# Kernel optimization log

Measured on AMD Instinct MI355X. Metric: run time of the kernel, lower is better.

The kernel has to match this reference:

```python
import jax, jax.numpy as jnp
import numpy as np

NEG_INF = -1e30

def _rotate_half(x):
    x1, x2 = jnp.split(x, 2, axis=-1)
    return jnp.concatenate([-x2, x1], axis=-1)

def _apply_rope(x, sin, cos):
    # x: [b, t, h, d]; sin/cos: [t, d]
    s = sin[None, :, None, :]
    c = cos[None, :, None, :]
    return x * c + _rotate_half(x) * s

def setup_inputs() -> dict:
    key = jax.random.key(0)
    ks = jax.random.split(key, 5)
    B, T, D, H = 2, 2048, 2048, 16
    hd = D // H
    x = jax.random.normal(ks[0], (B, T, D), dtype=jnp.float32)
    sin = jax.random.normal(ks[1], (T, hd), dtype=jnp.float32)
    cos = jax.random.normal(ks[2], (T, hd), dtype=jnp.float32)
    W_qkv = jax.random.normal(ks[3], (D, D + 2 * hd), dtype=jnp.float32) * (1.0 / np.sqrt(D))
    W_o = jax.random.normal(ks[4], (D, D), dtype=jnp.float32) * (1.0 / np.sqrt(D))
    return {"x": x, "sin": sin, "cos": cos, "W_qkv": W_qkv, "W_o": W_o}

def reference(x, sin, cos, W_qkv, W_o):
    B, T, D = x.shape
    num_heads = 16
    head_dim = D // num_heads
    scale = head_dim ** (-0.5)

    qkv = x @ W_qkv                              # [B, T, D + 2*hd]
    q, k, v = jnp.split(qkv, [D, D + head_dim], axis=-1)
    # q -> [B, H, T, hd]; k, v single KV head -> [B, 1, T, hd]
    q = q.reshape(B, T, num_heads, head_dim).transpose(0, 2, 1, 3)
    k = k[:, :, None, :].transpose(0, 2, 1, 3)   # [B, 1, T, hd]
    v = v[:, :, None, :].transpose(0, 2, 1, 3)

    # module scales q by head_dim^-0.5 BEFORE rope/attention
    q = q * scale

    # apply_rope_safe: transpose to [B, T, H, hd], apply rope, transpose back
    q = _apply_rope(q.transpose(0, 2, 1, 3), sin, cos).transpose(0, 2, 1, 3)
    k = _apply_rope(k.transpose(0, 2, 1, 3), sin, cos).transpose(0, 2, 1, 3)

    k0 = k[:, 0]                                 # [B, T, hd] (MQA shared KV)
    v0 = v[:, 0]

    # jax.nn.dot_product_attention applies its own 1/sqrt(hd) scaling on top
    scores = jnp.einsum('bhqd,bkd->bhqk', q, k0) * scale
    causal = jnp.tril(jnp.ones((T, T), dtype=bool))
    scores = jnp.where(causal[None, None], scores, NEG_INF)
    probs = jax.nn.softmax(scores, axis=-1)
    out = jnp.einsum('bhqk,bkd->bhqd', probs, v0)  # [B, H, T, hd]

    out = out.transpose(0, 2, 1, 3).reshape(B, T, D)
    return out @ W_o
```

## Files before the change

### kernel.cpp

```cpp
#include <hip/hip_runtime.h>
#include <stdint.h>

typedef __bf16 bf16x8_t __attribute__((ext_vector_type(8)));
typedef float f32x4_t __attribute__((ext_vector_type(4)));

#define AS1 __attribute__((address_space(1)))
#define AS3 __attribute__((address_space(3)))

static __device__ __forceinline__ unsigned short f2bf(float f) {
  union { float f; unsigned u; } a;
  a.f = f;
  unsigned r = a.u + 0x7fffu + ((a.u >> 16) & 1u);
  return (unsigned short)(r >> 16);
}

static __device__ __forceinline__ unsigned cvtpk(float lo, float hi) {
  unsigned r;
  asm("v_cvt_pk_bf16_f32 %0, %1, %2" : "=v"(r) : "v"(lo), "v"(hi));
  return r;
}

__global__ void cvt_bf16_kernel(const float* __restrict__ in, unsigned short* __restrict__ out) {
  long i = ((long)blockIdx.x * blockDim.x + threadIdx.x) * 4;
  float4 v = *(const float4*)(in + i);
  ushort4 o;
  o.x = f2bf(v.x);
  o.y = f2bf(v.y);
  o.z = f2bf(v.z);
  o.w = f2bf(v.w);
  *(ushort4*)(out + i) = o;
}

__global__ void transpose_f32_bf16(const float* __restrict__ src, unsigned short* __restrict__ dst,
                                   int ld, int dld, long sbs, long dbs) {
  __shared__ float tile[64][65];
  src += (long)blockIdx.z * sbs;
  dst += (long)blockIdx.z * dbs;
  const int c0 = blockIdx.x * 64, r0 = blockIdx.y * 64;
  const int tx = threadIdx.x, ty = threadIdx.y;
#pragma unroll
  for (int j = 0; j < 64; j += 4)
    tile[ty + j][tx] = src[(long)(r0 + ty + j) * ld + (c0 + tx)];
  __syncthreads();
#pragma unroll
  for (int j = 0; j < 64; j += 4)
    dst[(long)(c0 + ty + j) * dld + (r0 + tx)] = f2bf(tile[tx][ty + j]);
}

__global__ __launch_bounds__(256) void gemm_bt(const unsigned short* __restrict__ A,
                                               const unsigned short* __restrict__ Bt,
                                               float* __restrict__ C,
                                               int M, int N, int K, int nx) {
  __shared__ unsigned short As[3][128 * 32];
  __shared__ unsigned short Bs[3][128 * 32];
  const int nwg = gridDim.x;
  const int bid = blockIdx.x;
  const int swz = (bid & 7) * (nwg >> 3) + (bid >> 3);
  const int by = swz / nx;
  const int bx = swz - by * nx;

  const int tid = threadIdx.x;
  const int wid = tid >> 6, lane = tid & 63;
  const int r16 = lane & 15, g = lane >> 4;
  const long bm = (long)by * 128;
  const long bn = (long)bx * 128;
  const int wr = (wid >> 1) * 64, wc = (wid & 1) * 64;
  const int gr = g ^ (r16 & 3);
  const int sslot = (lane & 3) ^ ((lane >> 2) & 3);

  f32x4_t acc[4][4];
#pragma unroll
  for (int i = 0; i < 4; i++)
#pragma unroll
    for (int j = 0; j < 4; j++) acc[i][j] = (f32x4_t){0.f, 0.f, 0.f, 0.f};

  const int NT = K >> 5;

#define STAGE_G(buf, kt)                                                              \
  {                                                                                   \
    _Pragma("unroll") for (int i = 0; i < 2; i++) {                                   \
      const int chunk = (i * 4 + wid) * 64 + lane;                                    \
      const int row = chunk >> 2;                                                     \
      __builtin_amdgcn_global_load_lds(                                               \
          (const AS1 void*)(A + (bm + row) * K + (kt) + sslot * 8),                   \
          (AS3 void*)(&As[buf][chunk * 8]), 16, 0, 0);                                \
      __builtin_amdgcn_global_load_lds(                                               \
          (const AS1 void*)(Bt + (bn + row) * K + (kt) + sslot * 8),                  \
          (AS3 void*)(&Bs[buf][chunk * 8]), 16, 0, 0);                                \
    }                                                                                 \
  }

  STAGE_G(0, 0)
  STAGE_G(1, 32)
  asm volatile("s_waitcnt vmcnt(4)" ::: "memory");
  __builtin_amdgcn_s_barrier();

  for (int T = 0; T < NT; T++) {
    const int cur = T % 3;
    if (T + 2 < NT) {
      const int nb = (T + 2) % 3;
      STAGE_G(nb, (T + 2) * 32)
    }
    __builtin_amdgcn_sched_barrier(0);
    bf16x8_t af[4], bfr[4];
#pragma unroll
    for (int mi = 0; mi < 4; mi++)
      af[mi] = *(const bf16x8_t*)(&As[cur][(wr + mi * 16 + r16) * 32 + gr * 8]);
#pragma unroll
    for (int ni = 0; ni < 4; ni++)
      bfr[ni] = *(const bf16x8_t*)(&Bs[cur][(wc + ni * 16 + r16) * 32 + gr * 8]);
    __builtin_amdgcn_s_setprio(1);
#pragma unroll
    for (int mi = 0; mi < 4; mi++)
#pragma unroll
      for (int ni = 0; ni < 4; ni++)
        acc[mi][ni] = __builtin_amdgcn_mfma_f32_16x16x32_bf16(af[mi], bfr[ni], acc[mi][ni], 0, 0, 0);
    __builtin_amdgcn_s_setprio(0);
    if (T + 2 < NT)
      asm volatile("s_waitcnt vmcnt(4)" ::: "memory");
    else
      asm volatile("s_waitcnt vmcnt(0)" ::: "memory");
    __builtin_amdgcn_s_barrier();
  }
#undef STAGE_G

#pragma unroll
  for (int mi = 0; mi < 4; mi++)
#pragma unroll
    for (int ni = 0; ni < 4; ni++) {
      const long rowb = bm + wr + mi * 16 + 4 * g;
      const long colb = bn + wc + ni * 16 + r16;
#pragma unroll
      for (int j = 0; j < 4; j++)
        C[(rowb + j) * N + colb] = acc[mi][ni][j];
    }
}

__global__ void rope_kernel(const float* __restrict__ qkv,
                            const float* __restrict__ sinp,
                            const float* __restrict__ cosp,
                            unsigned short* __restrict__ qr,
                            unsigned short* __restrict__ kr) {
  const int row = blockIdx.x;
  const int b = row >> 11, t = row & 2047;
  const float* src = qkv + (long)row * 2304;
  const int tid = threadIdx.x;
  const int d = tid & 127;
  const int dp = (d + 64) & 127;
  const float c = cosp[t * 128 + d];
  const float s = sinp[t * 128 + d];
  const float sgn = (d < 64) ? -1.f : 1.f;
  for (int h = (tid >> 7); h < 16; h += 2) {
    const float x0 = src[h * 128 + d];
    const float xp = src[h * 128 + dp];
    qr[((long)((b * 16 + h) * 2048 + t)) * 128 + d] =
        f2bf((x0 * c + sgn * xp * s) * 0.011271055f);
  }
  if (tid < 128) {
    const float x0 = src[2048 + d];
    const float xp = src[2048 + dp];
    kr[((long)(b * 2048 + t)) * 128 + d] = f2bf(x0 * c + sgn * xp * s);
  }
}

__global__ __launch_bounds__(256, 2)
void mqa_attn(const unsigned short* __restrict__ qr,
              const unsigned short* __restrict__ kr,
              const unsigned short* __restrict__ vT,
              unsigned short* __restrict__ ao) {
  __shared__ unsigned short Kb[2][64 * 128];
  __shared__ unsigned short Vb[2][128 * 64];
  __shared__ unsigned short plds[4][16 * 64];
  const int idx = blockIdx.x;
  const int pj = idx & 15, h = (idx >> 4) & 15, b = idx >> 8;
  const int tid = threadIdx.x;
  const int wid = tid >> 6, lane = tid & 63;
  const int r = lane & 15, g = lane >> 4;
  const int rs = r & 7;
  char* pw = (char*)&plds[wid][0];

  const unsigned short* kbase = kr + (long)b * 2048 * 128;
  const unsigned short* vbase = vT + (long)b * 128 * 2048;
  const unsigned short* qh = qr + (long)(b * 16 + h) * 2048 * 128;

  const int scol = (tid & 15) ^ ((tid >> 4) & 7);
  const int vscol = (tid & 7) ^ ((tid >> 3) & 7);

  f32x4_t o[8];
#pragma unroll
  for (int i = 0; i < 8; i++) o[i] = (f32x4_t){0.f, 0.f, 0.f, 0.f};
  float m = 0.f, lsum = 0.f;

  int tile = pj;
  bf16x8_t qf[4];
  {
    const unsigned short* qp = qh + (long)(tile * 64 + wid * 16 + r) * 128 + g * 8;
#pragma unroll
    for (int c = 0; c < 4; c++) qf[c] = *(const bf16x8_t*)(qp + c * 32);
  }

#pragma unroll
  for (int i = 0; i < 4; i++) {
    const int row = i * 16 + (tid >> 4);
    __builtin_amdgcn_global_load_lds(
        (const AS1 void*)(kbase + (long)row * 128 + scol * 8),
        (AS3 void*)(&Kb[0][(i * 256 + tid) * 8]), 16, 0, 0);
  }
#pragma unroll
  for (int i = 0; i < 4; i++) {
    const int vrow = i * 32 + (tid >> 3);
    __builtin_amdgcn_global_load_lds(
        (const AS1 void*)(vbase + (long)vrow * 2048 + vscol * 8),
        (AS3 void*)(&Vb[0][(i * 256 + tid) * 8]), 16, 0, 0);
  }
  asm volatile("s_waitcnt vmcnt(0)" ::: "memory");
  __builtin_amdgcn_s_barrier();

  const int switch_s = pj + 1;
  for (int s = 0; s <= 32; s++) {
    const int cur = s & 1;

    if (s == switch_s) {
      float lt = lsum;
      lt += __shfl_xor(lt, 16);
      lt += __shfl_xor(lt, 32);
      float rl[4];
#pragma unroll
      for (int jj = 0; jj < 4; jj++) rl[jj] = 1.0f / __shfl(lt, 4 * g + jj);
      unsigned short* aop = ao + ((long)(b * 2048 + tile * 64 + wid * 16 + 4 * g)) * 2048 + h * 128 + r;
#pragma unroll
      for (int dt = 0; dt < 8; dt++)
#pragma unroll
        for (int jj = 0; jj < 4; jj++)
          aop[(long)jj * 2048 + dt * 16] = f2bf(o[dt][jj] * rl[jj]);
      tile = 31 - pj;
      const unsigned short* qp = qh + (long)(tile * 64 + wid * 16 + r) * 128 + g * 8;
#pragma unroll
      for (int c = 0; c < 4; c++) qf[c] = *(const bf16x8_t*)(qp + c * 32);
#pragma unroll
      for (int i = 0; i < 8; i++) o[i] = (f32x4_t){0.f, 0.f, 0.f, 0.f};
      m = 0.f;
      lsum = 0.f;
    }

    if (s < 32) {
      const int kvn = (s + 1 <= pj) ? 64 * (s + 1) : 64 * (s - pj);
#pragma unroll
      for (int i = 0; i < 4; i++) {
        const int row = i * 16 + (tid >> 4);
        __builtin_amdgcn_global_load_lds(
            (const AS1 void*)(kbase + (long)(kvn + row) * 128 + scol * 8),
            (AS3 void*)(&Kb[cur ^ 1][(i * 256 + tid) * 8]), 16, 0, 0);
      }
      __builtin_amdgcn_sched_barrier(0);
#pragma unroll
      for (int i = 0; i < 4; i++) {
        const int vrow = i * 32 + (tid >> 3);
        __builtin_amdgcn_global_load_lds(
            (const AS1 void*)(vbase + (long)vrow * 2048 + kvn + vscol * 8),
            (AS3 void*)(&Vb[cur ^ 1][(i * 256 + tid) * 8]), 16, 0, 0);
      }
    }
    __builtin_amdgcn_sched_barrier(0);

    f32x4_t sc[4];
#pragma unroll
    for (int t = 0; t < 4; t++) sc[t] = (f32x4_t){0.f, 0.f, 0.f, 0.f};
    const unsigned short* Kcur = &Kb[cur][0];
    __builtin_amdgcn_s_setprio(1);
#pragma unroll
    for (int t = 0; t < 4; t++) {
      const unsigned short* krow = Kcur + (16 * t + r) * 128;
#pragma unroll
      for (int c = 0; c < 4; c++) {
        const bf16x8_t kf = *(const bf16x8_t*)(krow + (((4 * c + g) ^ rs) << 3));
        sc[t] = __builtin_amdgcn_mfma_f32_16x16x32_bf16(kf, qf[c], sc[t], 0, 0, 0);
      }
    }
    __builtin_amdgcn_s_setprio(0);

    if (s == pj || s == 32) {
#pragma unroll
      for (int t = 0; t < 4; t++)
#pragma unroll
        for (int jj = 0; jj < 4; jj++)
          if (t * 16 + 4 * g + jj > wid * 16 + r) sc[t][jj] = -1e30f;
    }
    float mx01 = fmaxf(fmaxf(sc[0][0], sc[0][1]), fmaxf(sc[0][2], sc[0][3]));
    float mx23 = fmaxf(fmaxf(sc[1][0], sc[1][1]), fmaxf(sc[1][2], sc[1][3]));
    float mx45 = fmaxf(fmaxf(sc[2][0], sc[2][1]), fmaxf(sc[2][2], sc[2][3]));
    float mx67 = fmaxf(fmaxf(sc[3][0], sc[3][1]), fmaxf(sc[3][2], sc[3][3]));
    const float lm = fmaxf(fmaxf(mx01, mx23), fmaxf(mx45, mx67));
    if (!__all(lm <= m + 11.5f)) {
      float pm = lm;
      pm = fmaxf(pm, __shfl_xor(pm, 16));
      pm = fmaxf(pm, __shfl_xor(pm, 32));
      const float mnew = fmaxf(m, pm);
      const float alpha = __builtin_amdgcn_exp2f(m - mnew);
      lsum *= alpha;
      float aj[4];
#pragma unroll
      for (int jj = 0; jj < 4; jj++) aj[jj] = __shfl(alpha, 4 * g + jj);
#pragma unroll
      for (int dt = 0; dt < 8; dt++) {
        o[dt][0] *= aj[0]; o[dt][1] *= aj[1]; o[dt][2] *= aj[2]; o[dt][3] *= aj[3];
      }
      m = mnew;
    }
    float p[16];
#pragma unroll
    for (int t = 0; t < 4; t++)
#pragma unroll
      for (int jj = 0; jj < 4; jj++) p[4 * t + jj] = __builtin_amdgcn_exp2f(sc[t][jj] - m);
    float ls = 0.f;
#pragma unroll
    for (int i = 0; i < 16; i++) ls += p[i];
    lsum += ls;

    asm volatile("" ::: "memory");
#pragma unroll
    for (int t = 0; t < 4; t++) {
      uint2 w = {cvtpk(p[4 * t], p[4 * t + 1]), cvtpk(p[4 * t + 2], p[4 * t + 3])};
      *(uint2*)(pw + r * 128 + (((2 * t + (g >> 1)) ^ rs) << 4) + ((g & 1) << 3)) = w;
    }
    asm volatile("s_waitcnt lgkmcnt(0)" ::: "memory");
    const bf16x8_t pa0 = *(const bf16x8_t*)(pw + r * 128 + ((g ^ rs) << 4));
    const bf16x8_t pa1 = *(const bf16x8_t*)(pw + r * 128 + (((4 + g) ^ rs) << 4));

    if (s < 32)
      asm volatile("s_waitcnt vmcnt(8)" ::: "memory");
    else
      asm volatile("s_waitcnt vmcnt(0)" ::: "memory");
    __builtin_amdgcn_s_barrier();

    const unsigned short* Vcur = &Vb[cur][0];
    __builtin_amdgcn_s_setprio(1);
#pragma unroll
    for (int dt = 0; dt < 8; dt++) {
      const bf16x8_t vfA = *(const bf16x8_t*)(Vcur + (dt * 16 + r) * 64 + ((g ^ rs) << 3));
      o[dt] = __builtin_amdgcn_mfma_f32_16x16x32_bf16(pa0, vfA, o[dt], 0, 0, 0);
    }
#pragma unroll
    for (int dt = 0; dt < 8; dt++) {
      const bf16x8_t vfB = *(const bf16x8_t*)(Vcur + (dt * 16 + r) * 64 + (((4 + g) ^ rs) << 3));
      o[dt] = __builtin_amdgcn_mfma_f32_16x16x32_bf16(pa1, vfB, o[dt], 0, 0, 0);
    }
    __builtin_amdgcn_s_setprio(0);

    if (s < 32)
      asm volatile("s_waitcnt vmcnt(4)" ::: "memory");
    else
      asm volatile("s_waitcnt vmcnt(0)" ::: "memory");
    __builtin_amdgcn_s_barrier();
  }
  {
    float lt = lsum;
    lt += __shfl_xor(lt, 16);
    lt += __shfl_xor(lt, 32);
    float rl[4];
#pragma unroll
    for (int jj = 0; jj < 4; jj++) rl[jj] = 1.0f / __shfl(lt, 4 * g + jj);
    unsigned short* aop = ao + ((long)(b * 2048 + tile * 64 + wid * 16 + 4 * g)) * 2048 + h * 128 + r;
#pragma unroll
    for (int dt = 0; dt < 8; dt++)
#pragma unroll
      for (int jj = 0; jj < 4; jj++)
        aop[(long)jj * 2048 + dt * 16] = f2bf(o[dt][jj] * rl[jj]);
  }
}

extern "C" void kernel_launch(void* const* d_in, const int* in_sizes, int n_in,
                              void* d_out, int out_size, void* d_ws, size_t ws_size,
                              hipStream_t stream) {
  const float* x    = (const float*)d_in[0];
  const float* sinp = (const float*)d_in[1];
  const float* cosp = (const float*)d_in[2];
  const float* Wqkv = (const float*)d_in[3];
  const float* Wo   = (const float*)d_in[4];
  float* out = (float*)d_out;
  char* ws = (char*)d_ws;

  const int B = 2, T = 2048, D = 2048, H = 16, HD = 128;
  const int M = B * T;
  const int NQ = D + 2 * HD;

  unsigned short* xb    = (unsigned short*)(ws + 0);
  unsigned short* wqkvT = (unsigned short*)(ws + 16777216);
  unsigned short* woT   = (unsigned short*)(ws + 26214400);
  float*          qkv   = (float*)         (ws + 34603008);
  unsigned short* qr    = (unsigned short*)(ws + 72351744);
  unsigned short* kr    = (unsigned short*)(ws + 89128960);
  unsigned short* vT    = (unsigned short*)(ws + 90177536);
  unsigned short* ao    = xb;

  dim3 tb(64, 4);
  cvt_bf16_kernel<<<(M * D) / 1024, 256, 0, stream>>>(x, xb);
  transpose_f32_bf16<<<dim3(NQ / 64, D / 64, 1), tb, 0, stream>>>(Wqkv, wqkvT, NQ, D, 0, 0);
  transpose_f32_bf16<<<dim3(D / 64, D / 64, 1), tb, 0, stream>>>(Wo, woT, D, D, 0, 0);
  gemm_bt<<<dim3((NQ / 128) * (M / 128)), 256, 0, stream>>>(xb, wqkvT, qkv, M, NQ, D, NQ / 128);
  rope_kernel<<<M, 256, 0, stream>>>(qkv, sinp, cosp, qr, kr);
  transpose_f32_bf16<<<dim3(HD / 64, T / 64, B), tb, 0, stream>>>(
      qkv + 2176, vT, NQ, T, (long)T * NQ, (long)HD * T);
  mqa_attn<<<dim3(512), 256, 0, stream>>>(qr, kr, vT, ao);
  gemm_bt<<<dim3((D / 128) * (M / 128)), 256, 0, stream>>>(ao, woT, out, M, D, D, D / 128);
}
```

Baseline: 202.8 us.

## Fuse RoPE, scaling and V transpose into the QKV GEMM epilogue

The QKV projection GEMM now applies RoPE and the q scale in its epilogue, with each warp's column mapping paired so d and d+64 live in the same thread. It writes bf16 q/k directly and a transposed bf16 V through an LDS staging tile. This removes the fp32 qkv intermediate round trip plus the separate rope and V-transpose launches. It adds an interleaved cos/sin table kernel and a heavier epilogue with scattered float2 table reads.

```diff
diff --git a/kernel.cpp b/kernel.cpp
--- a/kernel.cpp
+++ b/kernel.cpp
@@ -18,6 +18,15 @@
   unsigned r;
   asm("v_cvt_pk_bf16_f32 %0, %1, %2" : "=v"(r) : "v"(lo), "v"(hi));
   return r;
+}
+
+__global__ void build_cs(const float* __restrict__ sinp, const float* __restrict__ cosp,
+                         float2* __restrict__ cs) {
+  const int i = blockIdx.x * 256 + threadIdx.x;
+  float2 v;
+  v.x = cosp[i];
+  v.y = sinp[i];
+  cs[i] = v;
 }
 
 __global__ void cvt_bf16_kernel(const float* __restrict__ in, unsigned short* __restrict__ out) {
@@ -46,6 +55,20 @@
   for (int j = 0; j < 64; j += 4)
     dst[(long)(c0 + ty + j) * dld + (r0 + tx)] = f2bf(tile[tx][ty + j]);
 }
+
+#define STAGE_G(Abase, Bbase, buf, kt)                                                \
+  {                                                                                   \
+    _Pragma("unroll") for (int i = 0; i < 2; i++) {                                   \
+      const int chunk = (i * 4 + wid) * 64 + lane;                                    \
+      const int row = chunk >> 2;                                                     \
+      __builtin_amdgcn_global_load_lds(                                               \
+          (const AS1 void*)(A + (bm + row) * K + (kt) + sslot * 8),                   \
+          (AS3 void*)(Abase + buf * 4096 + chunk * 8), 16, 0, 0);                     \
+      __builtin_amdgcn_global_load_lds(                                               \
+          (const AS1 void*)(Bt + (bn + row) * K + (kt) + sslot * 8),                  \
+          (AS3 void*)(Bbase + buf * 4096 + chunk * 8), 16, 0, 0);                     \
+    }                                                                                 \
+  }
 
 __global__ __launch_bounds__(256) void gemm_bt(const unsigned short* __restrict__ A,
                                                const unsigned short* __restrict__ Bt,
@@ -75,23 +98,11 @@
     for (int j = 0; j < 4; j++) acc[i][j] = (f32x4_t){0.f, 0.f, 0.f, 0.f};
 
   const int NT = K >> 5;
-
-#define STAGE_G(buf, kt)                                                              \
-  {                                                                                   \
-    _Pragma("unroll") for (int i = 0; i < 2; i++) {                                   \
-      const int chunk = (i * 4 + wid) * 64 + lane;                                    \
-      const int row = chunk >> 2;                                                     \
-      __builtin_amdgcn_global_load_lds(                                               \
-          (const AS1 void*)(A + (bm + row) * K + (kt) + sslot * 8),                   \
-          (AS3 void*)(&As[buf][chunk * 8]), 16, 0, 0);                                \
-      __builtin_amdgcn_global_load_lds(                                               \
-          (const AS1 void*)(Bt + (bn + row) * K + (kt) + sslot * 8),                  \
-          (AS3 void*)(&Bs[buf][chunk * 8]), 16, 0, 0);                                \
-    }                                                                                 \
-  }
-
-  STAGE_G(0, 0)
-  STAGE_G(1, 32)
+  unsigned short* Ab = &As[0][0];
+  unsigned short* Bb = &Bs[0][0];
+
+  STAGE_G(Ab, Bb, 0, 0)
+  STAGE_G(Ab, Bb, 1, 32)
   asm volatile("s_waitcnt vmcnt(4)" ::: "memory");
   __builtin_amdgcn_s_barrier();
 
@@ -99,16 +110,16 @@
     const int cur = T % 3;
     if (T + 2 < NT) {
       const int nb = (T + 2) % 3;
-      STAGE_G(nb, (T + 2) * 32)
+      STAGE_G(Ab, Bb, nb, (T + 2) * 32)
     }
     __builtin_amdgcn_sched_barrier(0);
     bf16x8_t af[4], bfr[4];
 #pragma unroll
     for (int mi = 0; mi < 4; mi++)
-      af[mi] = *(const bf16x8_t*)(&As[cur][(wr + mi * 16 + r16) * 32 + gr * 8]);
+      af[mi] = *(const bf16x8_t*)(Ab + cur * 4096 + (wr + mi * 16 + r16) * 32 + gr * 8);
 #pragma unroll
     for (int ni = 0; ni < 4; ni++)
-      bfr[ni] = *(const bf16x8_t*)(&Bs[cur][(wc + ni * 16 + r16) * 32 + gr * 8]);
+      bfr[ni] = *(const bf16x8_t*)(Bb + cur * 4096 + (wc + ni * 16 + r16) * 32 + gr * 8);
     __builtin_amdgcn_s_setprio(1);
 #pragma unroll
     for (int mi = 0; mi < 4; mi++)
@@ -122,7 +133,6 @@
       asm volatile("s_waitcnt vmcnt(0)" ::: "memory");
     __builtin_amdgcn_s_barrier();
   }
-#undef STAGE_G
 
 #pragma unroll
   for (int mi = 0; mi < 4; mi++)
@@ -136,30 +146,122 @@
     }
 }
 
-__global__ void rope_kernel(const float* __restrict__ qkv,
-                            const float* __restrict__ sinp,
-                            const float* __restrict__ cosp,
-                            unsigned short* __restrict__ qr,
-                            unsigned short* __restrict__ kr) {
-  const int row = blockIdx.x;
-  const int b = row >> 11, t = row & 2047;
-  const float* src = qkv + (long)row * 2304;
+__global__ __launch_bounds__(256) void gemm_qkv_rope(
+    const unsigned short* __restrict__ A,
+    const unsigned short* __restrict__ Bt,
+    const float2* __restrict__ cs,
+    unsigned short* __restrict__ qr,
+    unsigned short* __restrict__ kr,
+    unsigned short* __restrict__ vT) {
+  __shared__ unsigned short smem[6][128 * 32];
+  const int K = 2048, nx = 18, nwg = 576;
+  const int bid = blockIdx.x;
+  const int swz = (bid & 7) * (nwg >> 3) + (bid >> 3);
+  const int by = swz / nx;
+  const int bx = swz - by * nx;
+
   const int tid = threadIdx.x;
-  const int d = tid & 127;
-  const int dp = (d + 64) & 127;
-  const float c = cosp[t * 128 + d];
-  const float s = sinp[t * 128 + d];
-  const float sgn = (d < 64) ? -1.f : 1.f;
-  for (int h = (tid >> 7); h < 16; h += 2) {
-    const float x0 = src[h * 128 + d];
-    const float xp = src[h * 128 + dp];
-    qr[((long)((b * 16 + h) * 2048 + t)) * 128 + d] =
-        f2bf((x0 * c + sgn * xp * s) * 0.011271055f);
-  }
-  if (tid < 128) {
-    const float x0 = src[2048 + d];
-    const float xp = src[2048 + dp];
-    kr[((long)(b * 2048 + t)) * 128 + d] = f2bf(x0 * c + sgn * xp * s);
+  const int wid = tid >> 6, lane = tid & 63;
+  const int r16 = lane & 15, g = lane >> 4;
+  const long bm = (long)by * 128;
+  const long bn = (long)bx * 128;
+  const int wr = (wid >> 1) * 64;
+  const int wcp = (wid & 1) * 32;
+  const int gr = g ^ (r16 & 3);
+  const int sslot = (lane & 3) ^ ((lane >> 2) & 3);
+  const int colmap[4] = {0, 16, 64, 80};
+
+  f32x4_t acc[4][4];
+#pragma unroll
+  for (int i = 0; i < 4; i++)
+#pragma unroll
+    for (int j = 0; j < 4; j++) acc[i][j] = (f32x4_t){0.f, 0.f, 0.f, 0.f};
+
+  const int NT = K >> 5;
+  unsigned short* Ab = &smem[0][0];
+  unsigned short* Bb = &smem[3][0];
+
+  STAGE_G(Ab, Bb, 0, 0)
+  STAGE_G(Ab, Bb, 1, 32)
+  asm volatile("s_waitcnt vmcnt(4)" ::: "memory");
+  __builtin_amdgcn_s_barrier();
+
+  for (int T = 0; T < NT; T++) {
+    const int cur = T % 3;
+    if (T + 2 < NT) {
+      const int nb = (T + 2) % 3;
+      STAGE_G(Ab, Bb, nb, (T + 2) * 32)
+    }
+    __builtin_amdgcn_sched_barrier(0);
+    bf16x8_t af[4], bfr[4];
+#pragma unroll
+    for (int mi = 0; mi < 4; mi++)
+      af[mi] = *(const bf16x8_t*)(Ab + cur * 4096 + (wr + mi * 16 + r16) * 32 + gr * 8);
+#pragma unroll
+    for (int ni = 0; ni < 4; ni++)
+      bfr[ni] = *(const bf16x8_t*)(Bb + cur * 4096 + (wcp + colmap[ni] + r16) * 32 + gr * 8);
+    __builtin_amdgcn_s_setprio(1);
+#pragma unroll
+    for (int mi = 0; mi < 4; mi++)
+#pragma unroll
+      for (int ni = 0; ni < 4; ni++)
+        acc[mi][ni] = __builtin_amdgcn_mfma_f32_16x16x32_bf16(af[mi], bfr[ni], acc[mi][ni], 0, 0, 0);
+    __builtin_amdgcn_s_setprio(0);
+    if (T + 2 < NT)
+      asm volatile("s_waitcnt vmcnt(4)" ::: "memory");
+    else
+      asm volatile("s_waitcnt vmcnt(0)" ::: "memory");
+    __builtin_amdgcn_s_barrier();
+  }
+  const int b = by >> 4;
+  const int tseq0 = (by & 15) * 128;
+  unsigned short* sm = &smem[0][0];
+
+  if (bx < 17) {
+    const bool isq = (bx < 16);
+#pragma unroll
+    for (int mi = 0; mi < 4; mi++) {
+#pragma unroll
+      for (int ni = 0; ni < 4; ni++) {
+        const int d = wcp + colmap[ni] + r16;
+        const float sgn = (ni < 2) ? -1.f : 1.f;
+#pragma unroll
+        for (int j = 0; j < 4; j++) {
+          const int tl = wr + mi * 16 + 4 * g + j;
+          const float2 c = cs[(long)(tseq0 + tl) * 128 + d];
+          float v = acc[mi][ni][j] * c.x + sgn * acc[mi][ni ^ 2][j] * c.y;
+          if (isq) v *= 0.011271055f;
+          sm[tl * 136 + d] = f2bf(v);
+        }
+      }
+    }
+    __syncthreads();
+    const int trow = tid >> 1, half = (tid & 1) * 64;
+    unsigned short* dst =
+        isq ? (qr + ((long)(b * 16 + bx) * 2048 + tseq0) * 128)
+            : (kr + ((long)b * 2048 + tseq0) * 128);
+    dst += (long)trow * 128 + half;
+#pragma unroll
+    for (int i = 0; i < 8; i++)
+      *(bf16x8_t*)(dst + i * 8) = *(const bf16x8_t*)(sm + trow * 136 + half + i * 8);
+  } else {
+#pragma unroll
+    for (int mi = 0; mi < 4; mi++)
+#pragma unroll
+      for (int ni = 0; ni < 4; ni++) {
+        const int d = wcp + colmap[ni] + r16;
+#pragma unroll
+        for (int j = 0; j < 4; j++) {
+          const int tl = wr + mi * 16 + 4 * g + j;
+          sm[d * 136 + tl] = f2bf(acc[mi][ni][j]);
+        }
+      }
+    __syncthreads();
+    const int drow = tid >> 1, half = (tid & 1) * 64;
+    unsigned short* dst = vT + (long)b * 128 * 2048 + (long)drow * 2048 + tseq0 + half;
+#pragma unroll
+    for (int i = 0; i < 8; i++)
+      *(bf16x8_t*)(dst + i * 8) = *(const bf16x8_t*)(sm + drow * 136 + half + i * 8);
   }
 }
 
@@ -387,20 +489,18 @@
   unsigned short* xb    = (unsigned short*)(ws + 0);
   unsigned short* wqkvT = (unsigned short*)(ws + 16777216);
   unsigned short* woT   = (unsigned short*)(ws + 26214400);
-  float*          qkv   = (float*)         (ws + 34603008);
-  unsigned short* qr    = (unsigned short*)(ws + 72351744);
-  unsigned short* kr    = (unsigned short*)(ws + 89128960);
-  unsigned short* vT    = (unsigned short*)(ws + 90177536);
+  float2*         cstab = (float2*)        (ws + 34603008);
+  unsigned short* qr    = (unsigned short*)(ws + 36700160);
+  unsigned short* kr    = (unsigned short*)(ws + 53477376);
+  unsigned short* vT    = (unsigned short*)(ws + 54525952);
   unsigned short* ao    = xb;
 
   dim3 tb(64, 4);
+  build_cs<<<(T * HD) / 256, 256, 0, stream>>>(sinp, cosp, cstab);
   cvt_bf16_kernel<<<(M * D) / 1024, 256, 0, stream>>>(x, xb);
   transpose_f32_bf16<<<dim3(NQ / 64, D / 64, 1), tb, 0, stream>>>(Wqkv, wqkvT, NQ, D, 0, 0);
   transpose_f32_bf16<<<dim3(D / 64, D / 64, 1), tb, 0, stream>>>(Wo, woT, D, D, 0, 0);
-  gemm_bt<<<dim3((NQ / 128) * (M / 128)), 256, 0, stream>>>(xb, wqkvT, qkv, M, NQ, D, NQ / 128);
-  rope_kernel<<<M, 256, 0, stream>>>(qkv, sinp, cosp, qr, kr);
-  transpose_f32_bf16<<<dim3(HD / 64, T / 64, B), tb, 0, stream>>>(
-      qkv + 2176, vT, NQ, T, (long)T * NQ, (long)HD * T);
+  gemm_qkv_rope<<<dim3((NQ / 128) * (M / 128)), 256, 0, stream>>>(xb, wqkvT, cstab, qr, kr, vT);
   mqa_attn<<<dim3(512), 256, 0, stream>>>(qr, kr, vT, ao);
   gemm_bt<<<dim3((D / 128) * (M / 128)), 256, 0, stream>>>(ao, woT, out, M, D, D, D / 128);
 }
```

Measured after the change: 208.5 us. 1.03x slower.
